# Kernel optimization log

Measured on AMD Instinct MI355X. Metric: run time of the kernel, lower is better.

## Reference

```python
import jax, jax.numpy as jnp
import numpy as np


def setup_inputs() -> dict:
    key = jax.random.key(0)
    k1, k2, k3 = jax.random.split(key, 3)
    D, N, K = 512, 131072, 64
    x = jax.random.normal(k1, (D, N), dtype=jnp.float32)
    a_bar = jax.random.uniform(k2, (K, N), dtype=jnp.float32)
    c = jax.random.normal(k3, (K, D), dtype=jnp.float32)
    return {"x": x, "a_bar": a_bar, "c": c}


def reference(x, a_bar, c):
    # V[k, d] = sum_n a_bar[k, n] * (x[d, n] - c[k, d])
    #         = (a_bar @ x.T)[k, d] - c[k, d] * sum_n a_bar[k, n]
    # Fused form: one GEMM + one row-sum, never materializing (K, D, N) residuals.
    ax = jnp.einsum('kn,dn->kd', a_bar, x)        # (K, D)
    a_sum = jnp.sum(a_bar, axis=1, keepdims=True)  # (K, 1)
    V = ax - c * a_sum                              # (K, D)
    return V
```

## Files before the change

### kernel.cpp

```cpp
#include <hip/hip_runtime.h>
#include <hip/hip_bf16.h>


#define K_ROWS 64
#define D_COLS 512
#define N_RED  131072LL

#define DT     256
#define BK     32
#define XBYTES (DT * BK * 4)
#define ABYTES (K_ROWS * BK * 4)
#define BUFB   (XBYTES + ABYTES)

typedef __attribute__((ext_vector_type(8))) short short8;
typedef __attribute__((ext_vector_type(4))) float f32x4;

__device__ __forceinline__ short f2bf(float f) {
    __bf16 h = (__bf16)f;
    return __builtin_bit_cast(short, h);
}

__device__ __forceinline__ short8 cvt8(float4 a, float4 b) {
    short8 r;
    r[0] = f2bf(a.x); r[1] = f2bf(a.y); r[2] = f2bf(a.z); r[3] = f2bf(a.w);
    r[4] = f2bf(b.x); r[5] = f2bf(b.y); r[6] = f2bf(b.z); r[7] = f2bf(b.w);
    return r;
}

__device__ __forceinline__ void gload_lds16(const float* g, char* l) {
    __builtin_amdgcn_global_load_lds(
        (const __attribute__((address_space(1))) void*)g,
        (__attribute__((address_space(3))) void*)l, 16, 0, 0);
}

__device__ __forceinline__ void stage_tiles(
    const float* __restrict__ x, const float* __restrict__ ab,
    char* lbase, int d0, size_t noff, int tid)
{
    const int wb = tid & ~63;
    #pragma unroll
    for (int r = 0; r < 4; ++r) {
        int u   = r * 512 + tid;
        int row = u >> 3;
        int un  = (u & 7) ^ (row & 7);
        const float* g = x + (size_t)(d0 + row) * N_RED + noff + un * 4;
        gload_lds16(g, lbase + (size_t)(r * 512 + wb) * 16);
    }
    {
        int row = tid >> 3;
        int un  = (tid & 7) ^ (row & 7);
        const float* g = ab + (size_t)row * N_RED + noff + un * 4;
        gload_lds16(g, lbase + XBYTES + (size_t)wb * 16);
    }
}

__global__ __launch_bounds__(512, 4) void vlad_stage1(
    const float* __restrict__ x, const float* __restrict__ ab,
    float* __restrict__ pax, float* __restrict__ pasum, int chunk)
{
    extern __shared__ char smem[];
    const int g   = blockIdx.x & 1;
    const int s   = blockIdx.x >> 1;
    const int tid = threadIdx.x;
    const int w   = tid >> 6;
    const int l   = tid & 63;
    const int lr  = l & 15;
    const int lg  = l >> 4;
    const int d0  = g * DT;
    const size_t nblk = (size_t)s * chunk;
    const int steps   = chunk >> 5;
    const int swz     = lr & 7;

    int offx[2][2], offa[4][2];
    #pragma unroll
    for (int sub = 0; sub < 2; ++sub) {
        int xrow = w * 32 + sub * 16 + lr;
        #pragma unroll
        for (int c = 0; c < 2; ++c)
            offx[sub][c] = (xrow * 8 + ((lg * 2 + c) ^ swz)) * 16;
    }
    #pragma unroll
    for (int t = 0; t < 4; ++t) {
        int arow = t * 16 + lr;
        #pragma unroll
        for (int c = 0; c < 2; ++c)
            offa[t][c] = XBYTES + (arow * 8 + ((lg * 2 + c) ^ swz)) * 16;
    }

    f32x4 acc[4][2] = {};
    float asum[4] = {0.f, 0.f, 0.f, 0.f};
    const bool do_asum = (g == 0) && (w == 0);

    stage_tiles(x, ab, smem, d0, nblk, tid);

    int cur = 0;
    #pragma unroll 1
    for (int it = 0; it < steps; ++it) {
        __syncthreads();
        if (it + 1 < steps)
            stage_tiles(x, ab, smem + (cur ^ 1) * BUFB, d0,
                        nblk + (size_t)(it + 1) * BK, tid);

        char* b = smem + cur * BUFB;
        float4 a0[4], a1[4];
        #pragma unroll
        for (int t = 0; t < 4; ++t) {
            a0[t] = *(const float4*)(b + offa[t][0]);
            a1[t] = *(const float4*)(b + offa[t][1]);
        }
        float4 x0[2], x1[2];
        #pragma unroll
        for (int sub = 0; sub < 2; ++sub) {
            x0[sub] = *(const float4*)(b + offx[sub][0]);
            x1[sub] = *(const float4*)(b + offx[sub][1]);
        }
        if (do_asum) {
            #pragma unroll
            for (int t = 0; t < 4; ++t)
                asum[t] += ((a0[t].x + a0[t].y) + (a0[t].z + a0[t].w))
                         + ((a1[t].x + a1[t].y) + (a1[t].z + a1[t].w));
        }
        short8 xb0 = cvt8(x0[0], x1[0]);
        short8 xb1 = cvt8(x0[1], x1[1]);
        #pragma unroll
        for (int t = 0; t < 4; ++t) {
            short8 ab8 = cvt8(a0[t], a1[t]);
            acc[t][0] = __builtin_amdgcn_mfma_f32_16x16x32_bf16(ab8, xb0, acc[t][0], 0, 0, 0);
            acc[t][1] = __builtin_amdgcn_mfma_f32_16x16x32_bf16(ab8, xb1, acc[t][1], 0, 0, 0);
        }
        cur ^= 1;
    }

    float* dst = pax + (size_t)s * (K_ROWS * D_COLS);
    #pragma unroll
    for (int t = 0; t < 4; ++t)
        #pragma unroll
        for (int sub = 0; sub < 2; ++sub)
            #pragma unroll
            for (int r = 0; r < 4; ++r)
                dst[(size_t)(t * 16 + lg * 4 + r) * D_COLS
                    + d0 + w * 32 + sub * 16 + lr] = acc[t][sub][r];

    if (do_asum) {
        #pragma unroll
        for (int t = 0; t < 4; ++t) {
            asum[t] += __shfl_xor(asum[t], 16, 64);
            asum[t] += __shfl_xor(asum[t], 32, 64);
        }
        if (l < 16)
            #pragma unroll
            for (int t = 0; t < 4; ++t)
                pasum[s * K_ROWS + t * 16 + l] = asum[t];
    }
}

__global__ __launch_bounds__(256) void vlad_stage2(
    const float* __restrict__ pax, const float* __restrict__ pasum,
    const float* __restrict__ c, float* __restrict__ out, int S)
{
    __shared__ float red[256];
    __shared__ float ared[256];
    const int t  = threadIdx.x;
    const int o  = blockIdx.x * 64 + (t & 63);
    const int sp = t >> 6;
    const int k  = blockIdx.x >> 3;

    float pa = 0.f;
    for (int e = t; e < S; e += 256) pa += pasum[e * K_ROWS + k];
    ared[t] = pa;

    float acc = 0.f;
    for (int s = sp; s < S; s += 4)
        acc += pax[(size_t)s * (K_ROWS * D_COLS) + o];
    red[t] = acc;
    __syncthreads();

    for (int st = 128; st > 0; st >>= 1) {
        if (t < st) ared[t] += ared[t + st];
        __syncthreads();
    }
    if (sp == 0) {
        float v = red[t] + red[t + 64] + red[t + 128] + red[t + 192];
        out[o] = v - c[o] * ared[0];
    }
}

extern "C" void kernel_launch(void* const* d_in, const int* in_sizes, int n_in,
                              void* d_out, int out_size, void* d_ws, size_t ws_size,
                              hipStream_t stream)
{
    const float* x  = (const float*)d_in[0];
    const float* ab = (const float*)d_in[1];
    const float* c  = (const float*)d_in[2];
    float* out = (float*)d_out;

    int S = 256;
    while (S > 4 &&
           (size_t)S * (size_t)(K_ROWS * D_COLS + K_ROWS) * sizeof(float) > ws_size)
        S >>= 1;
    const int chunk = (int)(N_RED / S);

    float* pax   = (float*)d_ws;
    float* pasum = pax + (size_t)S * K_ROWS * D_COLS;

    vlad_stage1<<<dim3(2 * S), dim3(512), 2 * BUFB, stream>>>(x, ab, pax, pasum, chunk);
    vlad_stage2<<<dim3((K_ROWS * D_COLS) / 64), dim3(256), 0, stream>>>(pax, pasum, c, out, S);
}
```

Baseline: 81.80 us.

## Triple-buffer stage1 loads, store bf16 partials, remap blocks across XCDs

```diff
diff --git a/kernel.cpp b/kernel.cpp
--- a/kernel.cpp
+++ b/kernel.cpp
@@ -11,6 +11,7 @@
 #define XBYTES (DT * BK * 4)
 #define ABYTES (K_ROWS * BK * 4)
 #define BUFB   (XBYTES + ABYTES)
+#define NBUF   3
 
 typedef __attribute__((ext_vector_type(8))) short short8;
 typedef __attribute__((ext_vector_type(4))) float f32x4;
@@ -18,6 +19,10 @@
 __device__ __forceinline__ short f2bf(float f) {
     __bf16 h = (__bf16)f;
     return __builtin_bit_cast(short, h);
+}
+
+__device__ __forceinline__ float bf2f(unsigned short u) {
+    return __builtin_bit_cast(float, (unsigned)u << 16);
 }
 
 __device__ __forceinline__ short8 cvt8(float4 a, float4 b) {
@@ -33,75 +38,82 @@
         (__attribute__((address_space(3))) void*)l, 16, 0, 0);
 }
 
-__device__ __forceinline__ void stage_tiles(
+__global__ __launch_bounds__(512, 2) void vlad_stage1(
     const float* __restrict__ x, const float* __restrict__ ab,
-    char* lbase, int d0, size_t noff, int tid)
-{
-    const int wb = tid & ~63;
-    #pragma unroll
-    for (int r = 0; r < 4; ++r) {
-        int u   = r * 512 + tid;
-        int row = u >> 3;
-        int un  = (u & 7) ^ (row & 7);
-        const float* g = x + (size_t)(d0 + row) * N_RED + noff + un * 4;
-        gload_lds16(g, lbase + (size_t)(r * 512 + wb) * 16);
-    }
-    {
-        int row = tid >> 3;
-        int un  = (tid & 7) ^ (row & 7);
-        const float* g = ab + (size_t)row * N_RED + noff + un * 4;
-        gload_lds16(g, lbase + XBYTES + (size_t)wb * 16);
-    }
-}
-
-__global__ __launch_bounds__(512, 4) void vlad_stage1(
-    const float* __restrict__ x, const float* __restrict__ ab,
-    float* __restrict__ pax, float* __restrict__ pasum, int chunk)
+    unsigned short* __restrict__ pax, float* __restrict__ pasum, int chunk)
 {
     extern __shared__ char smem[];
-    const int g   = blockIdx.x & 1;
-    const int s   = blockIdx.x >> 1;
+    const int nwg     = gridDim.x;
+    const int cpx     = nwg >> 3;
+    const int logical = (blockIdx.x & 7) * cpx + (blockIdx.x >> 3);
+    const int g   = logical & 1;
+    const int s   = logical >> 1;
     const int tid = threadIdx.x;
     const int w   = tid >> 6;
     const int l   = tid & 63;
     const int lr  = l & 15;
     const int lg  = l >> 4;
     const int d0  = g * DT;
+    const int wb  = tid & ~63;
     const size_t nblk = (size_t)s * chunk;
     const int steps   = chunk >> 5;
     const int swz     = lr & 7;
 
+    const float* sg[5]; int sl[5];
+    #pragma unroll
+    for (int r2 = 0; r2 < 4; ++r2) {
+        int u = r2 * 512 + tid, row = u >> 3, un = (u & 7) ^ (row & 7);
+        sg[r2] = x + (size_t)(d0 + row) * N_RED + nblk + un * 4;
+        sl[r2] = (r2 * 512 + wb) * 16;
+    }
+    {
+        int row = tid >> 3, un = (tid & 7) ^ (row & 7);
+        sg[4] = ab + (size_t)row * N_RED + nblk + un * 4;
+        sl[4] = XBYTES + wb * 16;
+    }
+    auto stage = [&](int bi, int itn) {
+        char* base = smem + bi * BUFB;
+        #pragma unroll
+        for (int j = 0; j < 5; ++j)
+            gload_lds16(sg[j] + (size_t)itn * BK, base + sl[j]);
+    };
+
     int offx[2][2], offa[4][2];
     #pragma unroll
     for (int sub = 0; sub < 2; ++sub) {
         int xrow = w * 32 + sub * 16 + lr;
         #pragma unroll
-        for (int c = 0; c < 2; ++c)
-            offx[sub][c] = (xrow * 8 + ((lg * 2 + c) ^ swz)) * 16;
+        for (int cc = 0; cc < 2; ++cc)
+            offx[sub][cc] = (xrow * 8 + ((lg * 2 + cc) ^ swz)) * 16;
     }
     #pragma unroll
     for (int t = 0; t < 4; ++t) {
         int arow = t * 16 + lr;
         #pragma unroll
-        for (int c = 0; c < 2; ++c)
-            offa[t][c] = XBYTES + (arow * 8 + ((lg * 2 + c) ^ swz)) * 16;
+        for (int cc = 0; cc < 2; ++cc)
+            offa[t][cc] = XBYTES + (arow * 8 + ((lg * 2 + cc) ^ swz)) * 16;
     }
 
     f32x4 acc[4][2] = {};
     float asum[4] = {0.f, 0.f, 0.f, 0.f};
     const bool do_asum = (g == 0) && (w == 0);
 
-    stage_tiles(x, ab, smem, d0, nblk, tid);
+    stage(0, 0);
+    stage(1, 1);
 
     int cur = 0;
     #pragma unroll 1
     for (int it = 0; it < steps; ++it) {
-        __syncthreads();
-        if (it + 1 < steps)
-            stage_tiles(x, ab, smem + (cur ^ 1) * BUFB, d0,
-                        nblk + (size_t)(it + 1) * BK, tid);
-
-        char* b = smem + cur * BUFB;
+        if (it + 1 < steps) asm volatile("s_waitcnt vmcnt(5)" ::: "memory");
+        else                asm volatile("s_waitcnt vmcnt(0)" ::: "memory");
+        __builtin_amdgcn_s_barrier();
+        asm volatile("" ::: "memory");
+        if (it + 2 < steps) {
+            int nb = cur + 2; if (nb >= NBUF) nb -= NBUF;
+            stage(nb, it + 2);
+        }
+
+        const char* b = smem + cur * BUFB;
         float4 a0[4], a1[4];
         #pragma unroll
         for (int t = 0; t < 4; ++t) {
@@ -128,18 +140,19 @@
             acc[t][0] = __builtin_amdgcn_mfma_f32_16x16x32_bf16(ab8, xb0, acc[t][0], 0, 0, 0);
             acc[t][1] = __builtin_amdgcn_mfma_f32_16x16x32_bf16(ab8, xb1, acc[t][1], 0, 0, 0);
         }
-        cur ^= 1;
-    }
-
-    float* dst = pax + (size_t)s * (K_ROWS * D_COLS);
+        cur = (cur + 1 == NBUF) ? 0 : cur + 1;
+    }
+
+    unsigned short* dst = pax + (size_t)s * (K_ROWS * D_COLS);
     #pragma unroll
     for (int t = 0; t < 4; ++t)
         #pragma unroll
         for (int sub = 0; sub < 2; ++sub)
             #pragma unroll
-            for (int r = 0; r < 4; ++r)
-                dst[(size_t)(t * 16 + lg * 4 + r) * D_COLS
-                    + d0 + w * 32 + sub * 16 + lr] = acc[t][sub][r];
+            for (int r = 0; r < 4; ++r) {
+                int fg = (((g * 8 + w) * 4 + t) * 2 + sub) * 4 + r;
+                dst[fg * 64 + l] = (unsigned short)f2bf(acc[t][sub][r]);
+            }
 
     if (do_asum) {
         #pragma unroll
@@ -155,33 +168,41 @@
 }
 
 __global__ __launch_bounds__(256) void vlad_stage2(
-    const float* __restrict__ pax, const float* __restrict__ pasum,
+    const unsigned short* __restrict__ pax, const float* __restrict__ pasum,
     const float* __restrict__ c, float* __restrict__ out, int S)
 {
     __shared__ float red[256];
     __shared__ float ared[256];
     const int t  = threadIdx.x;
-    const int o  = blockIdx.x * 64 + (t & 63);
+    const int fo = t & 63;
     const int sp = t >> 6;
-    const int k  = blockIdx.x >> 3;
-
-    float pa = 0.f;
-    for (int e = t; e < S; e += 256) pa += pasum[e * K_ROWS + k];
-    ared[t] = pa;
+    const int fb = blockIdx.x * 64;
+    const int f  = fb + fo;
 
     float acc = 0.f;
     for (int s = sp; s < S; s += 4)
-        acc += pax[(size_t)s * (K_ROWS * D_COLS) + o];
+        acc += bf2f(pax[(size_t)s * (K_ROWS * D_COLS) + f]);
     red[t] = acc;
+
+    const int R = (fb >> 6) & 3, T = (fb >> 9) & 3;
+    const int ka = T * 16 + (t & 3) * 4 + R;
+    float pa = 0.f;
+    for (int s2 = t >> 2; s2 < S; s2 += 64)
+        pa += pasum[s2 * K_ROWS + ka];
+    ared[t] = pa;
     __syncthreads();
 
-    for (int st = 128; st > 0; st >>= 1) {
+    for (int st = 128; st >= 4; st >>= 1) {
         if (t < st) ared[t] += ared[t + st];
         __syncthreads();
     }
     if (sp == 0) {
+        int lr = f & 15, lg = (f >> 4) & 3, r = (f >> 6) & 3;
+        int sub = (f >> 8) & 1, tt = (f >> 9) & 3, w = (f >> 11) & 7, gg = (f >> 14) & 1;
+        int k = tt * 16 + lg * 4 + r;
+        int d = gg * 256 + w * 32 + sub * 16 + lr;
         float v = red[t] + red[t + 64] + red[t + 128] + red[t + 192];
-        out[o] = v - c[o] * ared[0];
+        out[k * D_COLS + d] = v - c[k * D_COLS + d] * ared[lg];
     }
 }
 
@@ -194,15 +215,15 @@
     const float* c  = (const float*)d_in[2];
     float* out = (float*)d_out;
 
-    int S = 256;
+    int S = 128;
     while (S > 4 &&
-           (size_t)S * (size_t)(K_ROWS * D_COLS + K_ROWS) * sizeof(float) > ws_size)
+           (size_t)S * ((size_t)K_ROWS * D_COLS * 2 + K_ROWS * 4) > ws_size)
         S >>= 1;
     const int chunk = (int)(N_RED / S);
 
-    float* pax   = (float*)d_ws;
-    float* pasum = pax + (size_t)S * K_ROWS * D_COLS;
-
-    vlad_stage1<<<dim3(2 * S), dim3(512), 2 * BUFB, stream>>>(x, ab, pax, pasum, chunk);
+    unsigned short* pax = (unsigned short*)d_ws;
+    float* pasum = (float*)((char*)d_ws + (size_t)S * K_ROWS * D_COLS * 2);
+
+    vlad_stage1<<<dim3(2 * S), dim3(512), NBUF * BUFB, stream>>>(x, ab, pax, pasum, chunk);
     vlad_stage2<<<dim3((K_ROWS * D_COLS) / 64), dim3(256), 0, stream>>>(pax, pasum, c, out, S);
 }
```

Result: slower. 89.23 us (+9.1%).
